# Kernel optimization log

Measured on AMD Instinct MI355X. Metric: run time of the kernel, lower is better.

## Reference

```python
import jax, jax.numpy as jnp
import numpy as np

EMBED_DIM = 1024
NUM_HEADS = 16
HEAD_DIM = EMBED_DIM // NUM_HEADS


def setup_inputs() -> dict:
    key = jax.random.key(0)
    ks = jax.random.split(key, 9)
    B, S, D = 2, 2048, EMBED_DIM
    scale = 1.0 / np.sqrt(D)
    inp = {
        "x": jax.random.normal(ks[0], (B, S, D), dtype=jnp.float32),
        "w_q": jax.random.normal(ks[1], (D, D), dtype=jnp.float32) * scale,
        "b_q": jnp.zeros((D,), dtype=jnp.float32),
        "w_k": jax.random.normal(ks[2], (D, D), dtype=jnp.float32) * scale,
        "b_k": jnp.zeros((D,), dtype=jnp.float32),
        "w_v": jax.random.normal(ks[3], (D, D), dtype=jnp.float32) * scale,
        "b_v": jnp.zeros((D,), dtype=jnp.float32),
        "w_o": jax.random.normal(ks[4], (D, D), dtype=jnp.float32) * scale,
        "b_o": jnp.zeros((D,), dtype=jnp.float32),
    }
    return inp


def reference(x, w_q, b_q, w_k, b_k, w_v, b_v, w_o, b_o):
    B, S, D = x.shape
    H, Hd = NUM_HEADS, HEAD_DIM

    def proj(w, b):
        # (B,S,D) @ (D,D) -> (B,S,D) -> (B,H,S,Hd)
        y = jnp.einsum('bsd,df->bsf', x, w) + b
        return y.reshape(B, S, H, Hd).transpose(0, 2, 1, 3)

    q = proj(w_q, b_q)
    k = proj(w_k, b_k)
    v = proj(w_v, b_v)

    scores = jnp.einsum('bhqd,bhkd->bhqk', q, k) / jnp.sqrt(jnp.float32(Hd))
    attn = jax.nn.softmax(scores, axis=-1)
    context = jnp.einsum('bhqk,bhkd->bhqd', attn, v)
    context = context.transpose(0, 2, 1, 3).reshape(B, S, D)
    return jnp.einsum('bsd,df->bsf', context + x, w_o) + b_o
```

## Files before the change

kernel.cpp:

```cpp
#include <hip/hip_runtime.h>
#include <hip/hip_bf16.h>

typedef _Float16 f16;
typedef _Float16 f16x8 __attribute__((ext_vector_type(8)));
typedef _Float16 f16x4 __attribute__((ext_vector_type(4)));
typedef float f32x4 __attribute__((ext_vector_type(4)));

#define EMBED 1024
#define NHEAD 16
#define HDIM 64
#define SEQ 2048
#define BATCH 2
#define NROW (BATCH * SEQ)
#define KBYTES 8192
#define WBYTES (2 * KBYTES)
#define OSTR 68
#define RBYTES ((64 * OSTR + 64) * 4)
#define MBIAS 14.4269504089f
#define QSCALE 0.1803368801f

__device__ __forceinline__ void gld_lds16(const f16* g, f16* l) {
    __builtin_amdgcn_global_load_lds(
        (const __attribute__((address_space(1))) void*)g,
        (__attribute__((address_space(3))) void*)l, 16, 0, 0);
}

__global__ void k_prep(const float* __restrict__ wq, const float* __restrict__ wk,
                       const float* __restrict__ wv, const float* __restrict__ wo,
                       const float* __restrict__ x,
                       const float* __restrict__ bq, const float* __restrict__ bk,
                       const float* __restrict__ bv,
                       f16* __restrict__ wqkvt, f16* __restrict__ wot, f16* __restrict__ xb,
                       float* __restrict__ bias) {
    if (blockIdx.z == 8) {
        int id = blockIdx.y * 32 + blockIdx.x;
        if (id < 12) {
            int i = id * 256 + threadIdx.x;
            bias[i] = (i < 1024) ? bq[i] : ((i < 2048) ? bk[i - 1024] : bv[i - 2048]);
        }
        return;
    }
    if (blockIdx.z >= 4) {
        int i = (((blockIdx.z - 4) * 1024 + blockIdx.y * 32 + blockIdx.x) * 256 + threadIdx.x) * 4;
        float4 v = *(const float4*)&x[i];
        f16x4 o = {(f16)v.x, (f16)v.y, (f16)v.z, (f16)v.w};
        *(f16x4*)&xb[i] = o;
        return;
    }
    const float* W;
    f16* Wt;
    switch (blockIdx.z) {
        case 0: W = wq; Wt = wqkvt; break;
        case 1: W = wk; Wt = wqkvt + 1024 * 1024; break;
        case 2: W = wv; Wt = wqkvt + 2 * 1024 * 1024; break;
        default: W = wo; Wt = wot; break;
    }
    __shared__ float t[32][33];
    int tx = threadIdx.x & 31, ty = threadIdx.x >> 5;
    int r0 = blockIdx.y * 32, c0 = blockIdx.x * 32;
    for (int j = 0; j < 4; ++j)
        t[ty + j * 8][tx] = W[(r0 + ty + j * 8) * 1024 + c0 + tx];
    __syncthreads();
    for (int j = 0; j < 4; ++j)
        Wt[(c0 + ty + j * 8) * 1024 + r0 + tx] = (f16)t[tx][ty + j * 8];
}

template <bool SWAP>
__device__ __forceinline__ void gemm_kloop64(const f16* __restrict__ A, const f16* __restrict__ Bt,
                                             int K, f16* Al, f16* Bl, int m0, int n0,
                                             int w, int quad, int l16, int mw, int nw,
                                             int crow2, int ccol2s, f32x4 (&acc)[4][4]) {
    int sw = l16 & 7;
    for (int k0 = 0; k0 < K; k0 += 64) {
        __syncthreads();
        for (int j = 0; j < 4; ++j) {
            gld_lds16(&A[(m0 + j * 32 + crow2) * K + k0 + ccol2s], &Al[(j * 32 + (w << 3)) * 64]);
            gld_lds16(&Bt[(n0 + j * 32 + crow2) * K + k0 + ccol2s], &Bl[(j * 32 + (w << 3)) * 64]);
        }
        __syncthreads();
        for (int kk = 0; kk < 2; ++kk) {
            f16x8 af[4], bf[4];
            for (int i = 0; i < 4; ++i)
                af[i] = *(const f16x8*)&Al[(mw + i * 16 + l16) * 64 + (((kk * 4 + quad) ^ sw) * 8)];
            for (int j = 0; j < 4; ++j)
                bf[j] = *(const f16x8*)&Bl[(nw + j * 16 + l16) * 64 + (((kk * 4 + quad) ^ sw) * 8)];
            for (int i = 0; i < 4; ++i)
                for (int j = 0; j < 4; ++j)
                    acc[i][j] = SWAP
                        ? __builtin_amdgcn_mfma_f32_16x16x32_f16(bf[j], af[i], acc[i][j], 0, 0, 0)
                        : __builtin_amdgcn_mfma_f32_16x16x32_f16(af[i], bf[j], acc[i][j], 0, 0, 0);
        }
    }
}

__global__ __launch_bounds__(256) void k_gemm_qkv(const f16* __restrict__ A, const f16* __restrict__ Bt,
                                                  const float* __restrict__ bias,
                                                  f16* __restrict__ qk, f16* __restrict__ Vt) {
    __shared__ __align__(16) f16 Al[128 * 64];
    __shared__ __align__(16) f16 Bl[128 * 64];
    const int K = 1024;
    int tid = threadIdx.x;
    int w = tid >> 6, lane = tid & 63, quad = lane >> 4, l16 = lane & 15;
    int m0 = blockIdx.x * 128, n0 = blockIdx.y * 128;
    int mw = (w >> 1) * 64, nw = (w & 1) * 64;
    int c = w * 64 + lane;
    int crow2 = c >> 3;
    int ccol2s = (((c & 7) ^ (crow2 & 7)) * 8);
    f32x4 acc[4][4] = {};

    if (n0 >= 2048) {
        gemm_kloop64<true>(A, Bt, K, Al, Bl, m0, n0, w, quad, l16, mw, nw, crow2, ccol2s, acc);
        for (int i = 0; i < 4; ++i) {
            int mrow = m0 + mw + i * 16 + l16;
            int b = mrow >> 11, s = mrow & 2047;
            for (int j = 0; j < 4; ++j)
                for (int r = 0; r < 4; ++r) {
                    int col = n0 + nw + j * 16 + quad * 4 + r;
                    int d = col - 2048;
                    Vt[(b * 1024 + d) * SEQ + s] = (f16)(acc[i][j][r] + bias[col]);
                }
        }
    } else {
        gemm_kloop64<false>(A, Bt, K, Al, Bl, m0, n0, w, quad, l16, mw, nw, crow2, ccol2s, acc);
        for (int i = 0; i < 4; ++i) {
            int row = m0 + mw + i * 16 + quad * 4;
            for (int j = 0; j < 4; ++j) {
                int col = n0 + nw + j * 16 + l16;
                float bval = bias[col];
                for (int r = 0; r < 4; ++r)
                    qk[(row + r) * 2048 + col] = (f16)(acc[i][j][r] + bval);
            }
        }
    }
}

__global__ __launch_bounds__(256) void k_gemm_out(const f16* __restrict__ A, const f16* __restrict__ Bt,
                                                  const float* __restrict__ bias, float* __restrict__ Cout) {
    __shared__ __align__(16) f16 Al[128 * 32];
    __shared__ __align__(16) f16 Bl[64 * 32];
    const int K = 1024, N = 1024;
    int tid = threadIdx.x;
    int w = tid >> 6, lane = tid & 63, quad = lane >> 4, l16 = lane & 15;
    int m0 = blockIdx.x * 128, n0 = blockIdx.y * 64;
    int mw = (w >> 1) * 64, nw = (w & 1) * 32;
    int c = w * 64 + lane;
    int crow = c >> 2, ccol = (c & 3) * 8;
    f32x4 acc[4][2] = {};

    for (int k0 = 0; k0 < K; k0 += 32) {
        __syncthreads();
        gld_lds16(&A[(m0 + crow) * K + k0 + ccol], &Al[(w * 64) * 8]);
        gld_lds16(&A[(m0 + 64 + crow) * K + k0 + ccol], &Al[(256 + w * 64) * 8]);
        gld_lds16(&Bt[(n0 + crow) * K + k0 + ccol], &Bl[(w * 64) * 8]);
        __syncthreads();
        f16x8 af[4], bf[2];
        for (int i = 0; i < 4; ++i)
            af[i] = *(const f16x8*)&Al[(mw + i * 16 + l16) * 32 + quad * 8];
        for (int j = 0; j < 2; ++j)
            bf[j] = *(const f16x8*)&Bl[(nw + j * 16 + l16) * 32 + quad * 8];
        for (int i = 0; i < 4; ++i)
            for (int j = 0; j < 2; ++j)
                acc[i][j] = __builtin_amdgcn_mfma_f32_16x16x32_f16(af[i], bf[j], acc[i][j], 0, 0, 0);
    }

    for (int i = 0; i < 4; ++i) {
        int row = m0 + mw + i * 16 + quad * 4;
        for (int j = 0; j < 2; ++j) {
            int col = n0 + nw + j * 16 + l16;
            float bval = bias[col];
            for (int r = 0; r < 4; ++r)
                Cout[(row + r) * N + col] = acc[i][j][r] + bval;
        }
    }
}

__global__ __launch_bounds__(256, 2) void k_attn(const f16* __restrict__ qk, const f16* __restrict__ Vt,
                                                 const float* __restrict__ x, f16* __restrict__ ctx) {
    __shared__ __align__(16) char smem[4 * WBYTES];

    int tid = threadIdx.x;
    int w = tid >> 6, lane = tid & 63, quad = lane >> 4, l16 = lane & 15;
    int q0 = blockIdx.x * 64;
    int bh = blockIdx.y, b = bh >> 4, h = bh & 15;
    int kbase = 1024 + h * 64;
    int qcol = h * 64;
    int vbase = b * 1024 + h * 64;

    f16* K0 = (f16*)(smem + w * WBYTES);
    f16* K1 = K0 + KBYTES / 2;

    int prow = lane >> 3;
    int pj = (lane & 7) ^ prow;
    const f16* kpre = &qk[(b * SEQ + w * 512 + prow) * 2048 + kbase + pj * 8];

    for (int c = 0; c < 8; ++c)
        gld_lds16(kpre + c * 8 * 2048, K0 + c * 512);
    kpre += 64 * 2048;

    f16x8 qf[4][2];
    for (int qg = 0; qg < 4; ++qg) {
        int qrow = b * SEQ + q0 + qg * 16 + l16;
        for (int kk = 0; kk < 2; ++kk) {
            f16x8 v = *(const f16x8*)&qk[qrow * 2048 + qcol + kk * 32 + quad * 8];
            for (int e = 0; e < 8; ++e) v[e] = (f16)((float)v[e] * QSCALE);
            qf[qg][kk] = v;
        }
    }

    const f16* vfp = &Vt[(vbase + l16) * SEQ + w * 512 + quad * 8];

    f32x4 oacc[4][4] = {};
    float li[4] = {0.f, 0.f, 0.f, 0.f};
    int sw = l16 & 7;

    f16* Kc = K0;
    f16* Kn = K1;
    for (int kt = 0; kt < 8; ++kt) {
        asm volatile("s_waitcnt vmcnt(0)" ::: "memory");

        f16x8 vr[4][2];
        for (int nt = 0; nt < 4; ++nt) {
            vr[nt][0] = *(const f16x8*)(vfp + nt * 16 * SEQ);
            vr[nt][1] = *(const f16x8*)(vfp + nt * 16 * SEQ + 32);
        }
        vfp += 64;

        f16x8 kf[4][2];
        for (int nt = 0; nt < 4; ++nt)
            for (int kk = 0; kk < 2; ++kk)
                kf[nt][kk] = *(const f16x8*)&Kc[(nt * 16 + l16) * 64 + (((kk * 4 + quad) ^ sw) * 8)];
        asm volatile("s_waitcnt lgkmcnt(0)" ::: "memory");

        if (kt < 7) {
            for (int c = 0; c < 8; ++c)
                gld_lds16(kpre + c * 8 * 2048, Kn + c * 512);
            kpre += 64 * 2048;
        }

        for (int qg = 0; qg < 4; ++qg) {
            f32x4 st[4];
            for (int nt = 0; nt < 4; ++nt) {
                f32x4 s = {};
                s = __builtin_amdgcn_mfma_f32_16x16x32_f16(kf[nt][0], qf[qg][0], s, 0, 0, 0);
                s = __builtin_amdgcn_mfma_f32_16x16x32_f16(kf[nt][1], qf[qg][1], s, 0, 0, 0);
                st[nt] = s;
            }
            float rs = 0.f;
            for (int nt = 0; nt < 4; ++nt)
                for (int r = 0; r < 4; ++r) {
                    float p = __builtin_amdgcn_exp2f(st[nt][r] - MBIAS);
                    st[nt][r] = p;
                    rs += p;
                }
            rs += __shfl_xor(rs, 16);
            rs += __shfl_xor(rs, 32);
            li[qg] += rs;
            int row = qg * 16 + l16;
            for (int nt = 0; nt < 4; ++nt) {
                f16x4 pk;
                for (int r = 0; r < 4; ++r) pk[r] = (f16)st[nt][r];
                *(f16x4*)&Kc[row * 64 + (((2 * nt + (quad >> 1)) ^ sw) * 8) + (quad & 1) * 4] = pk;
            }
        }
        asm volatile("s_waitcnt lgkmcnt(0)" ::: "memory");

        f16x8 pf[4][2];
        for (int qg = 0; qg < 4; ++qg)
            for (int kk = 0; kk < 2; ++kk)
                pf[qg][kk] = *(const f16x8*)&Kc[(qg * 16 + l16) * 64 + (((kk * 4 + quad) ^ sw) * 8)];
        for (int nt = 0; nt < 4; ++nt)
            for (int qg = 0; qg < 4; ++qg) {
                oacc[qg][nt] = __builtin_amdgcn_mfma_f32_16x16x32_f16(pf[qg][0], vr[nt][0], oacc[qg][nt], 0, 0, 0);
                oacc[qg][nt] = __builtin_amdgcn_mfma_f32_16x16x32_f16(pf[qg][1], vr[nt][1], oacc[qg][nt], 0, 0, 0);
            }
        f16* tmp = Kc; Kc = Kn; Kn = tmp;
    }

    float* Ow = (float*)(smem + (w & 1) * RBYTES);
    float* Lw = (float*)(smem + (w & 1) * RBYTES + 64 * OSTR * 4);
    __syncthreads();
    if (w < 2) {
        for (int qg = 0; qg < 4; ++qg)
            for (int nt = 0; nt < 4; ++nt)
                for (int r = 0; r < 4; ++r)
                    Ow[(qg * 16 + quad * 4 + r) * OSTR + nt * 16 + l16] = oacc[qg][nt][r];
        if (quad == 0)
            for (int qg = 0; qg < 4; ++qg) Lw[qg * 16 + l16] = li[qg];
    }
    __syncthreads();
    if (w >= 2) {
        for (int qg = 0; qg < 4; ++qg)
            for (int nt = 0; nt < 4; ++nt)
                for (int r = 0; r < 4; ++r)
                    Ow[(qg * 16 + quad * 4 + r) * OSTR + nt * 16 + l16] += oacc[qg][nt][r];
        if (quad == 0)
            for (int qg = 0; qg < 4; ++qg) Lw[qg * 16 + l16] += li[qg];
    }
    __syncthreads();

    int q = tid >> 2, d0 = (tid & 3) * 16;
    const float* O0 = (const float*)smem;
    const float* O1 = (const float*)(smem + RBYTES);
    f32x4 a4[4];
    for (int j = 0; j < 4; ++j)
        a4[j] = *(const f32x4*)&O0[q * OSTR + d0 + 4 * j];
    for (int j = 0; j < 4; ++j)
        a4[j] += *(const f32x4*)&O1[q * OSTR + d0 + 4 * j];
    float lsum = ((const float*)(smem + 64 * OSTR * 4))[q] +
                 ((const float*)(smem + RBYTES + 64 * OSTR * 4))[q];

    int g = b * SEQ + q0 + q;
    int cb = h * 64 + d0;
    float inv = 1.f / lsum;
    f16x8 o0, o1;
    for (int j = 0; j < 4; ++j) {
        float4 xv = *(const float4*)&x[g * 1024 + cb + 4 * j];
        float4 r;
        r.x = a4[j][0] * inv + xv.x;
        r.y = a4[j][1] * inv + xv.y;
        r.z = a4[j][2] * inv + xv.z;
        r.w = a4[j][3] * inv + xv.w;
        f16* dst = (j < 2) ? (f16*)&o0 : (f16*)&o1;
        int o = (j & 1) * 4;
        dst[o + 0] = (f16)r.x; dst[o + 1] = (f16)r.y; dst[o + 2] = (f16)r.z; dst[o + 3] = (f16)r.w;
    }
    *(f16x8*)&ctx[g * 1024 + cb] = o0;
    *(f16x8*)&ctx[g * 1024 + cb + 8] = o1;
}

extern "C" void kernel_launch(void* const* d_in, const int* in_sizes, int n_in,
                              void* d_out, int out_size, void* d_ws, size_t ws_size,
                              hipStream_t stream) {
    const float* x  = (const float*)d_in[0];
    const float* wq = (const float*)d_in[1];
    const float* bq = (const float*)d_in[2];
    const float* wk = (const float*)d_in[3];
    const float* bk = (const float*)d_in[4];
    const float* wv = (const float*)d_in[5];
    const float* bv = (const float*)d_in[6];
    const float* wo = (const float*)d_in[7];
    const float* bo = (const float*)d_in[8];
    float* out = (float*)d_out;

    char* ws = (char*)d_ws;
    f16*   xb    = (f16*)(ws);
    f16*   wqkvt = (f16*)(ws + (8u << 20));
    f16*   wot   = (f16*)(ws + (14u << 20));
    float* biasq = (float*)(ws + (16u << 20));
    f16*   qkbuf = (f16*)(ws + (16u << 20) + (64u << 10));
    f16*   vtbuf = (f16*)(ws + (32u << 20) + (64u << 10));
    f16*   ctx   = xb;

    k_prep<<<dim3(32, 32, 9), 256, 0, stream>>>(wq, wk, wv, wo, x, bq, bk, bv,
                                                wqkvt, wot, xb, biasq);

    k_gemm_qkv<<<dim3(32, 24), 256, 0, stream>>>(xb, wqkvt, biasq, qkbuf, vtbuf);
    k_attn<<<dim3(SEQ / 64, BATCH * NHEAD), 256, 0, stream>>>(qkbuf, vtbuf, x, ctx);
    k_gemm_out<<<dim3(32, 16), 256, 0, stream>>>(ctx, wot, bo, out);
}
```

Measured before the change: 203.9 us.

## Rewrite QKV GEMM as 256x256 tile with double-buffered async LDS pipeline

```diff
diff --git a/kernel.cpp b/kernel.cpp
--- a/kernel.cpp
+++ b/kernel.cpp
@@ -65,70 +65,125 @@
         Wt[(c0 + ty + j * 8) * 1024 + r0 + tx] = (f16)t[tx][ty + j * 8];
 }
 
-template <bool SWAP>
-__device__ __forceinline__ void gemm_kloop64(const f16* __restrict__ A, const f16* __restrict__ Bt,
-                                             int K, f16* Al, f16* Bl, int m0, int n0,
-                                             int w, int quad, int l16, int mw, int nw,
-                                             int crow2, int ccol2s, f32x4 (&acc)[4][4]) {
-    int sw = l16 & 7;
-    for (int k0 = 0; k0 < K; k0 += 64) {
-        __syncthreads();
-        for (int j = 0; j < 4; ++j) {
-            gld_lds16(&A[(m0 + j * 32 + crow2) * K + k0 + ccol2s], &Al[(j * 32 + (w << 3)) * 64]);
-            gld_lds16(&Bt[(n0 + j * 32 + crow2) * K + k0 + ccol2s], &Bl[(j * 32 + (w << 3)) * 64]);
-        }
-        __syncthreads();
-        for (int kk = 0; kk < 2; ++kk) {
-            f16x8 af[4], bf[4];
-            for (int i = 0; i < 4; ++i)
-                af[i] = *(const f16x8*)&Al[(mw + i * 16 + l16) * 64 + (((kk * 4 + quad) ^ sw) * 8)];
-            for (int j = 0; j < 4; ++j)
-                bf[j] = *(const f16x8*)&Bl[(nw + j * 16 + l16) * 64 + (((kk * 4 + quad) ^ sw) * 8)];
-            for (int i = 0; i < 4; ++i)
-                for (int j = 0; j < 4; ++j)
-                    acc[i][j] = SWAP
-                        ? __builtin_amdgcn_mfma_f32_16x16x32_f16(bf[j], af[i], acc[i][j], 0, 0, 0)
-                        : __builtin_amdgcn_mfma_f32_16x16x32_f16(af[i], bf[j], acc[i][j], 0, 0, 0);
-        }
-    }
-}
-
-__global__ __launch_bounds__(256) void k_gemm_qkv(const f16* __restrict__ A, const f16* __restrict__ Bt,
+__global__ __launch_bounds__(512) void k_gemm_qkv(const f16* __restrict__ A, const f16* __restrict__ Bt,
                                                   const float* __restrict__ bias,
                                                   f16* __restrict__ qk, f16* __restrict__ Vt) {
-    __shared__ __align__(16) f16 Al[128 * 64];
-    __shared__ __align__(16) f16 Bl[128 * 64];
-    const int K = 1024;
+    __shared__ __align__(16) f16 lds[2][4][8192];
     int tid = threadIdx.x;
-    int w = tid >> 6, lane = tid & 63, quad = lane >> 4, l16 = lane & 15;
-    int m0 = blockIdx.x * 128, n0 = blockIdx.y * 128;
-    int mw = (w >> 1) * 64, nw = (w & 1) * 64;
-    int c = w * 64 + lane;
-    int crow2 = c >> 3;
-    int ccol2s = (((c & 7) ^ (crow2 & 7)) * 8);
-    f32x4 acc[4][4] = {};
-
-    if (n0 >= 2048) {
-        gemm_kloop64<true>(A, Bt, K, Al, Bl, m0, n0, w, quad, l16, mw, nw, crow2, ccol2s, acc);
-        for (int i = 0; i < 4; ++i) {
-            int mrow = m0 + mw + i * 16 + l16;
-            int b = mrow >> 11, s = mrow & 2047;
-            for (int j = 0; j < 4; ++j)
-                for (int r = 0; r < 4; ++r) {
-                    int col = n0 + nw + j * 16 + quad * 4 + r;
-                    int d = col - 2048;
-                    Vt[(b * 1024 + d) * SEQ + s] = (f16)(acc[i][j][r] + bias[col]);
-                }
-        }
-    } else {
-        gemm_kloop64<false>(A, Bt, K, Al, Bl, m0, n0, w, quad, l16, mw, nw, crow2, ccol2s, acc);
-        for (int i = 0; i < 4; ++i) {
-            int row = m0 + mw + i * 16 + quad * 4;
-            for (int j = 0; j < 4; ++j) {
-                int col = n0 + nw + j * 16 + l16;
+    int wv = tid >> 6, lane = tid & 63, quad = lane >> 4, l16 = lane & 15;
+    int wm = wv >> 2, wn = wv & 3;
+    int m0 = blockIdx.x * 256, n0 = blockIdx.y * 256;
+    bool vpath = (n0 >= 2048);
+
+    int s0 = tid, s1 = 512 + tid;
+    int r0 = s0 >> 3, c0s = ((s0 & 7) ^ (r0 & 7)) * 8;
+    int r1 = s1 >> 3, c1s = ((s1 & 7) ^ (r1 & 7)) * 8;
+    int ldsb0 = (wv * 64) * 8;
+    int ldsb1 = (512 + wv * 64) * 8;
+
+#define STAGE(buf, reg, G, rowBase, kc) do { \
+    gld_lds16(&G[(rowBase + r0) * 1024 + (kc) + c0s], &lds[buf][reg][0] + ldsb0); \
+    gld_lds16(&G[(rowBase + r1) * 1024 + (kc) + c1s], &lds[buf][reg][0] + ldsb1); } while (0)
+
+    STAGE(0, 2, Bt, n0, 0);
+    STAGE(0, 3, Bt, n0 + 128, 0);
+    STAGE(0, 0, A, m0, 0);
+    STAGE(0, 1, A, m0 + 128, 0);
+    STAGE(1, 2, Bt, n0, 64);
+    STAGE(1, 3, Bt, n0 + 128, 64);
+    asm volatile("s_waitcnt vmcnt(4)" ::: "memory");
+    __builtin_amdgcn_s_barrier();
+
+    f32x4 acc[8][4] = {};
+    const int brow = (wn & 1) * 64;
+    const int breg = 2 + (wn >> 1);
+
+#pragma unroll 1
+    for (int it = 0; it < 8; ++it) {
+        int kc1 = (2 * it + 1) * 64, kc2 = (2 * it + 2) * 64, kc3 = (2 * it + 3) * 64;
+        f16x8 afr[4][2], bfr[2][2][2];
+#pragma unroll
+        for (int p = 0; p < 8; ++p) {
+            const int q = p & 3, buf = p >> 2;
+            const int mh = q >> 1;
+            const int nh = (q == 1 || q == 2) ? 1 : 0;
+            if (q == 0 || q == 2) {
+                for (int i = 0; i < 4; ++i)
+                    for (int kk = 0; kk < 2; ++kk) {
+                        int lr = mh * 64 + i * 16 + l16;
+                        afr[i][kk] = *(const f16x8*)&lds[buf][wm][lr * 64 + (((kk * 4 + quad) ^ (lr & 7)) * 8)];
+                    }
+            }
+            if (q == 0 || q == 1) {
+                for (int j = 0; j < 2; ++j)
+                    for (int kk = 0; kk < 2; ++kk) {
+                        int lr = brow + nh * 32 + j * 16 + l16;
+                        bfr[nh][j][kk] = *(const f16x8*)&lds[buf][breg][lr * 64 + (((kk * 4 + quad) ^ (lr & 7)) * 8)];
+                    }
+            }
+            switch (p) {
+                case 0: STAGE(1, 0, A, m0, kc1); break;
+                case 1: STAGE(1, 1, A, m0 + 128, kc1); break;
+                case 2: if (it < 7) STAGE(0, 2, Bt, n0, kc2); break;
+                case 3: if (it < 7) STAGE(0, 3, Bt, n0 + 128, kc2); break;
+                case 4: if (it < 7) STAGE(0, 0, A, m0, kc2); break;
+                case 5: if (it < 7) STAGE(0, 1, A, m0 + 128, kc2); break;
+                case 6: if (it < 7) STAGE(1, 2, Bt, n0, kc3); break;
+                case 7: if (it < 7) STAGE(1, 3, Bt, n0 + 128, kc3); break;
+            }
+            __builtin_amdgcn_s_barrier();
+            asm volatile("s_waitcnt lgkmcnt(0)" ::: "memory");
+            __builtin_amdgcn_s_setprio(1);
+            if (!vpath) {
+                for (int i = 0; i < 4; ++i)
+                    for (int j = 0; j < 2; ++j) {
+                        f32x4 a = acc[mh * 4 + i][nh * 2 + j];
+                        a = __builtin_amdgcn_mfma_f32_16x16x32_f16(afr[i][0], bfr[nh][j][0], a, 0, 0, 0);
+                        a = __builtin_amdgcn_mfma_f32_16x16x32_f16(afr[i][1], bfr[nh][j][1], a, 0, 0, 0);
+                        acc[mh * 4 + i][nh * 2 + j] = a;
+                    }
+            } else {
+                for (int i = 0; i < 4; ++i)
+                    for (int j = 0; j < 2; ++j) {
+                        f32x4 a = acc[mh * 4 + i][nh * 2 + j];
+                        a = __builtin_amdgcn_mfma_f32_16x16x32_f16(bfr[nh][j][0], afr[i][0], a, 0, 0, 0);
+                        a = __builtin_amdgcn_mfma_f32_16x16x32_f16(bfr[nh][j][1], afr[i][1], a, 0, 0, 0);
+                        acc[mh * 4 + i][nh * 2 + j] = a;
+                    }
+            }
+            __builtin_amdgcn_s_setprio(0);
+            if (p == 3) {
+                if (it < 7) asm volatile("s_waitcnt vmcnt(4)" ::: "memory");
+                else        asm volatile("s_waitcnt vmcnt(0)" ::: "memory");
+            }
+            if (p == 7 && it < 7)
+                asm volatile("s_waitcnt vmcnt(4)" ::: "memory");
+            __builtin_amdgcn_s_barrier();
+        }
+    }
+#undef STAGE
+
+    if (!vpath) {
+        for (int mi = 0; mi < 8; ++mi) {
+            int row = m0 + wm * 128 + mi * 16 + quad * 4;
+            for (int nj = 0; nj < 4; ++nj) {
+                int col = n0 + wn * 64 + nj * 16 + l16;
                 float bval = bias[col];
                 for (int r = 0; r < 4; ++r)
-                    qk[(row + r) * 2048 + col] = (f16)(acc[i][j][r] + bval);
+                    qk[(row + r) * 2048 + col] = (f16)(acc[mi][nj][r] + bval);
+            }
+        }
+    } else {
+        for (int mi = 0; mi < 8; ++mi) {
+            int mrow = m0 + wm * 128 + mi * 16 + l16;
+            int b = mrow >> 11, s = mrow & 2047;
+            for (int nj = 0; nj < 4; ++nj) {
+                int colb = n0 + wn * 64 + nj * 16 + quad * 4;
+                for (int r = 0; r < 4; ++r) {
+                    int col = colb + r;
+                    int d = col - 2048;
+                    Vt[(b * 1024 + d) * SEQ + s] = (f16)(acc[mi][nj][r] + bias[col]);
+                }
             }
         }
     }
@@ -354,7 +409,7 @@
     k_prep<<<dim3(32, 32, 9), 256, 0, stream>>>(wq, wk, wv, wo, x, bq, bk, bv,
                                                 wqkvt, wot, xb, biasq);
 
-    k_gemm_qkv<<<dim3(32, 24), 256, 0, stream>>>(xb, wqkvt, biasq, qkbuf, vtbuf);
+    k_gemm_qkv<<<dim3(16, 12), 512, 0, stream>>>(xb, wqkvt, biasq, qkbuf, vtbuf);
     k_attn<<<dim3(SEQ / 64, BATCH * NHEAD), 256, 0, stream>>>(qkbuf, vtbuf, x, ctx);
     k_gemm_out<<<dim3(32, 16), 256, 0, stream>>>(ctx, wot, bo, out);
 }
```

Measured after the change: 231.4 us. 13.5% more time.
